# Performance work log

Measured on AMD Instinct MI355X. Metric: run time of the kernel, lower is better.

The kernel has to match this reference:

```python
import jax, jax.numpy as jnp
import numpy as np

DIM = 1024
NUM_HEADS = 16
HEAD_DIM = DIM // NUM_HEADS
SCALE = HEAD_DIM ** -0.5


def setup_inputs() -> dict:
    key = jax.random.key(0)
    k1, k2, k3, k4 = jax.random.split(key, 4)
    x = jax.random.normal(k1, (4, 2048, DIM), dtype=jnp.float32)
    # torch nn.Linear(dim, 3*dim, bias=False): weight shape [3*dim, dim]
    w_qkv = jax.random.normal(k2, (3 * DIM, DIM), dtype=jnp.float32) * (DIM ** -0.5)
    # torch nn.Linear(dim, dim): weight [dim, dim], bias [dim]
    w_proj = jax.random.normal(k3, (DIM, DIM), dtype=jnp.float32) * (DIM ** -0.5)
    b_proj = jax.random.normal(k4, (DIM,), dtype=jnp.float32) * 0.01
    return {"x": x, "w_qkv": w_qkv, "w_proj": w_proj, "b_proj": b_proj}


def reference(x, w_qkv, w_proj, b_proj):
    B, N, C = x.shape
    # qkv: [B, N, 3*C] -> [3, B, H, N, Dh]
    qkv = (x @ w_qkv.T).reshape(B, N, 3, NUM_HEADS, HEAD_DIM)
    qkv = jnp.transpose(qkv, (2, 0, 3, 1, 4))
    q, k, v = qkv[0], qkv[1], qkv[2]
    # full score matrix, as in the original module
    attn = jnp.einsum("bhqd,bhkd->bhqk", q, k) * SCALE
    attn = jax.nn.softmax(attn, axis=-1)
    out = jnp.einsum("bhqk,bhkd->bhqd", attn, v)  # [B,H,N,Dh]
    out = jnp.transpose(out, (0, 2, 1, 3)).reshape(B, N, C)
    return out @ w_proj.T + b_proj
```

## Files before the change

kernel.cpp:

```cpp
#include <hip/hip_runtime.h>
#include <stdint.h>

#define DIM 1024
#define SEQ 2048
#define BATCH 4
#define ROWS (BATCH*SEQ)
#define QSCALE 0.1803368801111f

typedef __attribute__((ext_vector_type(8))) short bf16x8;
typedef __attribute__((ext_vector_type(4))) float f32x4;

#if __has_builtin(__builtin_amdgcn_exp2f)
#define EXP2F(x) __builtin_amdgcn_exp2f(x)
#else
#define EXP2F(x) __expf((x) * 0.69314718056f)
#endif

__device__ __forceinline__ unsigned short f2bf(float f) {
  union { float f; unsigned int u; } v; v.f = f;
  unsigned int u = v.u;
  return (unsigned short)((u + 0x7FFFu + ((u >> 16) & 1u)) >> 16);
}

__device__ __forceinline__ unsigned int pack_bf16_trunc(float lo, float hi) {
  union { float f; unsigned int u; } a, b;
  a.f = lo; b.f = hi;
  return __builtin_amdgcn_perm(b.u, a.u, 0x07060302u);
}

__device__ __forceinline__ void gload_lds16(const void* g, void* l) {
  __builtin_amdgcn_global_load_lds(
      (const __attribute__((address_space(1))) unsigned int*)g,
      (__attribute__((address_space(3))) unsigned int*)l,
      16, 0, 0);
}

__global__ void cast_f32_bf16(const float* __restrict__ src,
                              unsigned short* __restrict__ dst, int n) {
  int i = (blockIdx.x * blockDim.x + threadIdx.x) * 4;
  if (i < n) {
    float4 f = *(const float4*)(src + i);
    ushort4 o;
    o.x = f2bf(f.x); o.y = f2bf(f.y); o.z = f2bf(f.z); o.w = f2bf(f.w);
    *(ushort4*)(dst + i) = o;
  }
}

__global__ __launch_bounds__(256) void gemm_qkv(
    const unsigned short* __restrict__ A,
    const unsigned short* __restrict__ W,
    unsigned short* __restrict__ qb,
    unsigned short* __restrict__ kb,
    unsigned short* __restrict__ vtb) {
  const int K = DIM;
  __shared__ unsigned short Al[128 * 32];
  __shared__ unsigned short Wl[128 * 32];
  const int tid  = threadIdx.x;
  const int wave = tid >> 6, lane = tid & 63;
  const int quad = lane >> 4, l16 = lane & 15;
  const int m0 = blockIdx.y * 128, n0 = blockIdx.x * 128;
  const int wr = (wave >> 1) * 64, wc = (wave & 1) * 64;
  const int which = n0 >> 10;

  f32x4 acc[4][4];
#pragma unroll
  for (int i = 0; i < 4; i++)
#pragma unroll
    for (int j = 0; j < 4; j++) acc[i][j] = (f32x4)0.f;

  const int arow = wave * 16 + (lane >> 2);
  const int acol = (lane & 3) * 8;
  const unsigned short* Ag = A + (size_t)(m0 + arow) * K + acol;
  const unsigned short* Wg = W + (size_t)(n0 + arow) * K + acol;

  if (which < 2) {
    for (int kt = 0; kt < K; kt += 32) {
      __syncthreads();
#pragma unroll
      for (int i = 0; i < 2; i++) {
        gload_lds16((const void*)(Ag + (size_t)(i * 64) * K + kt), (void*)&Al[i * 2048 + wave * 512]);
        gload_lds16((const void*)(Wg + (size_t)(i * 64) * K + kt), (void*)&Wl[i * 2048 + wave * 512]);
      }
      __syncthreads();
      bf16x8 af[4], wf[4];
#pragma unroll
      for (int i = 0; i < 4; i++) {
        af[i] = *(const bf16x8*)&Al[(wr + i * 16 + l16) * 32 + quad * 8];
        wf[i] = *(const bf16x8*)&Wl[(wc + i * 16 + l16) * 32 + quad * 8];
      }
#pragma unroll
      for (int i = 0; i < 4; i++)
#pragma unroll
        for (int j = 0; j < 4; j++)
          acc[i][j] = __builtin_amdgcn_mfma_f32_16x16x32_bf16(wf[j], af[i], acc[i][j], 0, 0, 0);
    }
    const float sc = (which == 0) ? QSCALE : 1.f;
    unsigned short* base = (which == 0) ? qb : kb;
#pragma unroll
    for (int i = 0; i < 4; i++) {
      const int tok = m0 + wr + i * 16 + l16;
      const int b = tok >> 11, n = tok & 2047;
#pragma unroll
      for (int j = 0; j < 4; j++) {
        const int col0 = n0 + wc + j * 16 + quad * 4;
        const int h = (col0 >> 6) & 15, d = col0 & 63;
        ushort4 o4;
        o4.x = f2bf(acc[i][j][0] * sc); o4.y = f2bf(acc[i][j][1] * sc);
        o4.z = f2bf(acc[i][j][2] * sc); o4.w = f2bf(acc[i][j][3] * sc);
        *(ushort4*)&base[((size_t)(b * 16 + h) * SEQ + n) * 64 + d] = o4;
      }
    }
  } else {
    for (int kt = 0; kt < K; kt += 32) {
      __syncthreads();
#pragma unroll
      for (int i = 0; i < 2; i++) {
        gload_lds16((const void*)(Ag + (size_t)(i * 64) * K + kt), (void*)&Al[i * 2048 + wave * 512]);
        gload_lds16((const void*)(Wg + (size_t)(i * 64) * K + kt), (void*)&Wl[i * 2048 + wave * 512]);
      }
      __syncthreads();
      bf16x8 af[4], wf[4];
#pragma unroll
      for (int i = 0; i < 4; i++) {
        af[i] = *(const bf16x8*)&Al[(wr + i * 16 + l16) * 32 + quad * 8];
        wf[i] = *(const bf16x8*)&Wl[(wc + i * 16 + l16) * 32 + quad * 8];
      }
#pragma unroll
      for (int i = 0; i < 4; i++)
#pragma unroll
        for (int j = 0; j < 4; j++)
          acc[i][j] = __builtin_amdgcn_mfma_f32_16x16x32_bf16(af[i], wf[j], acc[i][j], 0, 0, 0);
    }
#pragma unroll
    for (int i = 0; i < 4; i++) {
      const int row = m0 + wr + i * 16 + quad * 4;
      const int b = row >> 11, n = row & 2047;
#pragma unroll
      for (int j = 0; j < 4; j++) {
        const int col = n0 + wc + j * 16 + l16;
        const int h = (col >> 6) & 15, d = col & 63;
        ushort4 o4;
        o4.x = f2bf(acc[i][j][0]); o4.y = f2bf(acc[i][j][1]);
        o4.z = f2bf(acc[i][j][2]); o4.w = f2bf(acc[i][j][3]);
        *(ushort4*)&vtb[((size_t)(b * 16 + h) * 64 + d) * SEQ + n] = o4;
      }
    }
  }
}

__global__ __launch_bounds__(256, 2) void attn_kernel(
    const unsigned short* __restrict__ qb,
    const unsigned short* __restrict__ kb,
    const unsigned short* __restrict__ vtb,
    unsigned short* __restrict__ out) {
  __shared__ unsigned short Kl[2][64 * 64];
  __shared__ unsigned short Vl[2][64 * 64];
  __shared__ unsigned short Pb[4][64 * 64];

  const int tid  = threadIdx.x;
  const int wave = tid >> 6, lane = tid & 63;
  const int quad = lane >> 4, l16 = lane & 15;
  const int qtile = blockIdx.x;
  const int bh    = blockIdx.y;
  const size_t qkbase = (size_t)bh * SEQ * 64;
  const int q0 = qtile * 256 + wave * 64;

  bf16x8 qf[4][2];
#pragma unroll
  for (int mi = 0; mi < 4; mi++)
#pragma unroll
    for (int kk = 0; kk < 2; kk++)
      qf[mi][kk] = *(const bf16x8*)&qb[qkbase + (size_t)(q0 + mi * 16 + l16) * 64 + kk * 32 + quad * 8];

  f32x4 o[4][4];
#pragma unroll
  for (int mi = 0; mi < 4; mi++)
#pragma unroll
    for (int nt = 0; nt < 4; nt++) o[mi][nt] = (f32x4)0.f;
  f32x4 lacc[4];
#pragma unroll
  for (int mi = 0; mi < 4; mi++) lacc[mi] = (f32x4)0.f;

  bf16x8 ones;
#pragma unroll
  for (int j = 0; j < 8; j++) ones[j] = (short)0x3F80;

  const unsigned short* Kg = kb + qkbase;
  const unsigned short* Vg = vtb + (size_t)bh * 64 * SEQ;
  const int srow = tid >> 3;
  const int schk = tid & 7;

  auto stage = [&](int kt, int buf) {
#pragma unroll
    for (int p = 0; p < 2; p++) {
      const int r = p * 32 + srow;
      const int sw = schk ^ (r & 7);
      gload_lds16((const void*)(Kg + (size_t)(kt + r) * 64 + sw * 8),
                  (void*)&Kl[buf][p * 2048 + wave * 512]);
      gload_lds16((const void*)(Vg + (size_t)r * SEQ + kt + sw * 8),
                  (void*)&Vl[buf][p * 2048 + wave * 512]);
    }
  };

  stage(0, 0);

  int buf = 0;
  for (int kt = 0; kt < SEQ; kt += 64, buf ^= 1) {
    __syncthreads();
    if (kt + 64 < SEQ) stage(kt + 64, buf ^ 1);

#pragma unroll
    for (int nh = 0; nh < 4; nh++) {
      const int R = nh * 16 + l16;
      const int sb = R & 7;
      bf16x8 kf0 = *(const bf16x8*)&Kl[buf][R * 64 + ((quad ^ sb) << 3)];
      bf16x8 kf1 = *(const bf16x8*)&Kl[buf][R * 64 + (((4 + quad) ^ sb) << 3)];
#pragma unroll
      for (int mi = 0; mi < 4; mi++) {
        f32x4 s = (f32x4)0.f;
        s = __builtin_amdgcn_mfma_f32_16x16x32_bf16(kf0, qf[mi][0], s, 0, 0, 0);
        s = __builtin_amdgcn_mfma_f32_16x16x32_bf16(kf1, qf[mi][1], s, 0, 0, 0);
        const float e0 = EXP2F(s[0]), e1 = EXP2F(s[1]);
        const float e2 = EXP2F(s[2]), e3 = EXP2F(s[3]);
        uint2 pk;
        pk.x = pack_bf16_trunc(e0, e1);
        pk.y = pack_bf16_trunc(e2, e3);
        const int q = mi * 16 + l16;
        const int chunk = (nh * 2 + (quad >> 1)) ^ (l16 & 7);
        *(uint2*)&Pb[wave][q * 64 + (chunk << 3) + ((quad & 1) << 2)] = pk;
      }
    }

#pragma unroll
    for (int kk = 0; kk < 2; kk++) {
      bf16x8 vf[4];
#pragma unroll
      for (int nt = 0; nt < 4; nt++) {
        const int R = nt * 16 + l16;
        vf[nt] = *(const bf16x8*)&Vl[buf][R * 64 + (((kk * 4 + quad) ^ (R & 7)) << 3)];
      }
#pragma unroll
      for (int mi = 0; mi < 4; mi++) {
        const int R = mi * 16 + l16;
        bf16x8 pf = *(const bf16x8*)&Pb[wave][R * 64 + (((kk * 4 + quad) ^ (l16 & 7)) << 3)];
        lacc[mi] = __builtin_amdgcn_mfma_f32_16x16x32_bf16(pf, ones, lacc[mi], 0, 0, 0);
#pragma unroll
        for (int nt = 0; nt < 4; nt++)
          o[mi][nt] = __builtin_amdgcn_mfma_f32_16x16x32_bf16(pf, vf[nt], o[mi][nt], 0, 0, 0);
      }
    }
  }

  const int h = bh & 15, b = bh >> 4;
#pragma unroll
  for (int mi = 0; mi < 4; mi++) {
    float inv[4];
#pragma unroll
    for (int r = 0; r < 4; r++) inv[r] = 1.f / lacc[mi][r];
#pragma unroll
    for (int nt = 0; nt < 4; nt++)
#pragma unroll
      for (int r = 0; r < 4; r++)
        out[((size_t)(b * SEQ + q0 + mi * 16 + quad * 4 + r)) * DIM + h * 64 + nt * 16 + l16] =
            f2bf(o[mi][nt][r] * inv[r]);
  }
}

__global__ __launch_bounds__(256) void gemm_proj(
    const unsigned short* __restrict__ A,
    const unsigned short* __restrict__ W,
    float* __restrict__ out,
    const float* __restrict__ bias) {
  const int N = DIM, K = DIM;
  __shared__ unsigned short Al[128 * 32];
  __shared__ unsigned short Wl[128 * 32];
  const int tid  = threadIdx.x;
  const int wave = tid >> 6, lane = tid & 63;
  const int quad = lane >> 4, l16 = lane & 15;
  const int m0 = blockIdx.y * 128, n0 = blockIdx.x * 128;
  const int wr = (wave >> 1) * 64, wc = (wave & 1) * 64;

  f32x4 acc[4][4];
#pragma unroll
  for (int i = 0; i < 4; i++)
#pragma unroll
    for (int j = 0; j < 4; j++) acc[i][j] = (f32x4)0.f;

  const int arow = wave * 16 + (lane >> 2);
  const int acol = (lane & 3) * 8;
  const unsigned short* Ag = A + (size_t)(m0 + arow) * K + acol;
  const unsigned short* Wg = W + (size_t)(n0 + arow) * K + acol;

  for (int kt = 0; kt < K; kt += 32) {
    __syncthreads();
#pragma unroll
    for (int i = 0; i < 2; i++) {
      gload_lds16((const void*)(Ag + (size_t)(i * 64) * K + kt), (void*)&Al[i * 2048 + wave * 512]);
      gload_lds16((const void*)(Wg + (size_t)(i * 64) * K + kt), (void*)&Wl[i * 2048 + wave * 512]);
    }
    __syncthreads();

    bf16x8 af[4], wf[4];
#pragma unroll
    for (int i = 0; i < 4; i++) {
      af[i] = *(const bf16x8*)&Al[(wr + i * 16 + l16) * 32 + quad * 8];
      wf[i] = *(const bf16x8*)&Wl[(wc + i * 16 + l16) * 32 + quad * 8];
    }
#pragma unroll
    for (int i = 0; i < 4; i++)
#pragma unroll
      for (int j = 0; j < 4; j++)
        acc[i][j] = __builtin_amdgcn_mfma_f32_16x16x32_bf16(af[i], wf[j], acc[i][j], 0, 0, 0);
  }

#pragma unroll
  for (int i = 0; i < 4; i++) {
    const int row = m0 + wr + i * 16 + quad * 4;
#pragma unroll
    for (int j = 0; j < 4; j++) {
      const int col = n0 + wc + j * 16 + l16;
      const float bv = bias[col];
#pragma unroll
      for (int r = 0; r < 4; r++)
        out[(size_t)(row + r) * N + col] = acc[i][j][r] + bv;
    }
  }
}

extern "C" void kernel_launch(void* const* d_in, const int* in_sizes, int n_in,
                              void* d_out, int out_size, void* d_ws, size_t ws_size,
                              hipStream_t stream) {
  const float* x      = (const float*)d_in[0];
  const float* w_qkv  = (const float*)d_in[1];
  const float* w_proj = (const float*)d_in[2];
  const float* b_proj = (const float*)d_in[3];
  float* outp = (float*)d_out;

  char* ws = (char*)d_ws;
  unsigned short* xb     = (unsigned short*)(ws);
  unsigned short* wqkvb  = (unsigned short*)(ws + (16u << 20));
  unsigned short* wprojb = (unsigned short*)(ws + (22u << 20));
  unsigned short* qb     = (unsigned short*)(ws + (24u << 20));
  unsigned short* kb     = (unsigned short*)(ws + (40u << 20));
  unsigned short* vtb    = (unsigned short*)(ws + (56u << 20));
  unsigned short* aout   = (unsigned short*)(ws + (72u << 20));

  cast_f32_bf16<<<ROWS * DIM / 1024, 256, 0, stream>>>(x, xb, ROWS * DIM);
  cast_f32_bf16<<<3 * DIM * DIM / 1024, 256, 0, stream>>>(w_qkv, wqkvb, 3 * DIM * DIM);
  cast_f32_bf16<<<DIM * DIM / 1024, 256, 0, stream>>>(w_proj, wprojb, DIM * DIM);

  gemm_qkv<<<dim3(24, 64), 256, 0, stream>>>(xb, wqkvb, qb, kb, vtb);
  attn_kernel<<<dim3(8, 64), 256, 0, stream>>>(qb, kb, vtb, aout);
  gemm_proj<<<dim3(8, 64), 256, 0, stream>>>(aout, wprojb, outp, b_proj);
}
```

Before: 266.2 us.

## Keep softmax probabilities in registers via fp16 MFMA and merge cast kernels

The attention kernel now feeds exp'd scores straight from the QK^T accumulator layout into 16x16x16 fp16 MFMAs for PV and the row sum, which removes the per-wave LDS P buffer and its store/load round trip. To make this work, V is stored as fp16 instead of bf16, and probabilities are packed with cvt_pkrtz. The three f32-to-bf16 cast launches are merged into one kernel. In exchange the PV MFMAs use half the K depth, so twice as many instructions are issued, and fp16 may overflow for large V values.

Result: slower. 281.0 us (+5.5%).

```diff
diff --git a/kernel.cpp b/kernel.cpp
--- a/kernel.cpp
+++ b/kernel.cpp
@@ -9,6 +9,8 @@
 
 typedef __attribute__((ext_vector_type(8))) short bf16x8;
 typedef __attribute__((ext_vector_type(4))) float f32x4;
+typedef __attribute__((ext_vector_type(4))) _Float16 f16x4;
+typedef __attribute__((ext_vector_type(2))) __fp16 fp16x2_raw;
 
 #if __has_builtin(__builtin_amdgcn_exp2f)
 #define EXP2F(x) __builtin_amdgcn_exp2f(x)
@@ -16,16 +18,24 @@
 #define EXP2F(x) __expf((x) * 0.69314718056f)
 #endif
 
+#define MFMA16x16(a,b,c) __builtin_amdgcn_mfma_f32_16x16x16f16(a,b,c,0,0,0)
+
 __device__ __forceinline__ unsigned short f2bf(float f) {
   union { float f; unsigned int u; } v; v.f = f;
   unsigned int u = v.u;
   return (unsigned short)((u + 0x7FFFu + ((u >> 16) & 1u)) >> 16);
 }
 
-__device__ __forceinline__ unsigned int pack_bf16_trunc(float lo, float hi) {
-  union { float f; unsigned int u; } a, b;
-  a.f = lo; b.f = hi;
-  return __builtin_amdgcn_perm(b.u, a.u, 0x07060302u);
+__device__ __forceinline__ unsigned short f2h(float f) {
+  union { _Float16 h; unsigned short u; } v;
+  v.h = (_Float16)f;
+  return v.u;
+}
+
+__device__ __forceinline__ unsigned int pkrtz_bits(float lo, float hi) {
+  union { fp16x2_raw h; unsigned int u; } v;
+  v.h = __builtin_amdgcn_cvt_pkrtz(lo, hi);
+  return v.u;
 }
 
 __device__ __forceinline__ void gload_lds16(const void* g, void* l) {
@@ -35,15 +45,23 @@
       16, 0, 0);
 }
 
-__global__ void cast_f32_bf16(const float* __restrict__ src,
-                              unsigned short* __restrict__ dst, int n) {
-  int i = (blockIdx.x * blockDim.x + threadIdx.x) * 4;
-  if (i < n) {
-    float4 f = *(const float4*)(src + i);
-    ushort4 o;
-    o.x = f2bf(f.x); o.y = f2bf(f.y); o.z = f2bf(f.z); o.w = f2bf(f.w);
-    *(ushort4*)(dst + i) = o;
-  }
+__global__ void cast_all(const float* __restrict__ x,
+                         const float* __restrict__ wq,
+                         const float* __restrict__ wp,
+                         unsigned short* __restrict__ xb,
+                         unsigned short* __restrict__ wqb,
+                         unsigned short* __restrict__ wpb) {
+  const int i = (blockIdx.x * blockDim.x + threadIdx.x) * 4;
+  const float* src;
+  unsigned short* dst;
+  int off;
+  if (i < ROWS * DIM)                 { src = x;  dst = xb;  off = i; }
+  else if (i < ROWS * DIM + 3 * DIM * DIM) { src = wq; dst = wqb; off = i - ROWS * DIM; }
+  else                                { src = wp; dst = wpb; off = i - ROWS * DIM - 3 * DIM * DIM; }
+  float4 f = *(const float4*)(src + off);
+  ushort4 o;
+  o.x = f2bf(f.x); o.y = f2bf(f.y); o.z = f2bf(f.z); o.w = f2bf(f.w);
+  *(ushort4*)(dst + off) = o;
 }
 
 __global__ __launch_bounds__(256) void gemm_qkv(
@@ -140,8 +158,8 @@
         const int col = n0 + wc + j * 16 + l16;
         const int h = (col >> 6) & 15, d = col & 63;
         ushort4 o4;
-        o4.x = f2bf(acc[i][j][0]); o4.y = f2bf(acc[i][j][1]);
-        o4.z = f2bf(acc[i][j][2]); o4.w = f2bf(acc[i][j][3]);
+        o4.x = f2h(acc[i][j][0]); o4.y = f2h(acc[i][j][1]);
+        o4.z = f2h(acc[i][j][2]); o4.w = f2h(acc[i][j][3]);
         *(ushort4*)&vtb[((size_t)(b * 16 + h) * 64 + d) * SEQ + n] = o4;
       }
     }
@@ -155,7 +173,6 @@
     unsigned short* __restrict__ out) {
   __shared__ unsigned short Kl[2][64 * 64];
   __shared__ unsigned short Vl[2][64 * 64];
-  __shared__ unsigned short Pb[4][64 * 64];
 
   const int tid  = threadIdx.x;
   const int wave = tid >> 6, lane = tid & 63;
@@ -181,9 +198,8 @@
 #pragma unroll
   for (int mi = 0; mi < 4; mi++) lacc[mi] = (f32x4)0.f;
 
-  bf16x8 ones;
-#pragma unroll
-  for (int j = 0; j < 8; j++) ones[j] = (short)0x3F80;
+  union { f16x4 v; unsigned int d[2]; } ones;
+  ones.d[0] = 0x3C003C00u; ones.d[1] = 0x3C003C00u;
 
   const unsigned short* Kg = kb + qkbase;
   const unsigned short* Vg = vtb + (size_t)bh * 64 * SEQ;
@@ -215,38 +231,25 @@
       const int sb = R & 7;
       bf16x8 kf0 = *(const bf16x8*)&Kl[buf][R * 64 + ((quad ^ sb) << 3)];
       bf16x8 kf1 = *(const bf16x8*)&Kl[buf][R * 64 + (((4 + quad) ^ sb) << 3)];
+      f16x4 vf[4];
+#pragma unroll
+      for (int nt = 0; nt < 4; nt++) {
+        const int vr = nt * 16 + l16;
+        const int c = nh * 2 + (quad >> 1);
+        vf[nt] = *(const f16x4*)&Vl[buf][vr * 64 + (((c ^ (vr & 7)) << 3) | ((quad & 1) << 2))];
+      }
 #pragma unroll
       for (int mi = 0; mi < 4; mi++) {
         f32x4 s = (f32x4)0.f;
         s = __builtin_amdgcn_mfma_f32_16x16x32_bf16(kf0, qf[mi][0], s, 0, 0, 0);
         s = __builtin_amdgcn_mfma_f32_16x16x32_bf16(kf1, qf[mi][1], s, 0, 0, 0);
-        const float e0 = EXP2F(s[0]), e1 = EXP2F(s[1]);
-        const float e2 = EXP2F(s[2]), e3 = EXP2F(s[3]);
-        uint2 pk;
-        pk.x = pack_bf16_trunc(e0, e1);
-        pk.y = pack_bf16_trunc(e2, e3);
-        const int q = mi * 16 + l16;
-        const int chunk = (nh * 2 + (quad >> 1)) ^ (l16 & 7);
-        *(uint2*)&Pb[wave][q * 64 + (chunk << 3) + ((quad & 1) << 2)] = pk;
-      }
-    }
-
-#pragma unroll
-    for (int kk = 0; kk < 2; kk++) {
-      bf16x8 vf[4];
-#pragma unroll
-      for (int nt = 0; nt < 4; nt++) {
-        const int R = nt * 16 + l16;
-        vf[nt] = *(const bf16x8*)&Vl[buf][R * 64 + (((kk * 4 + quad) ^ (R & 7)) << 3)];
-      }
-#pragma unroll
-      for (int mi = 0; mi < 4; mi++) {
-        const int R = mi * 16 + l16;
-        bf16x8 pf = *(const bf16x8*)&Pb[wave][R * 64 + (((kk * 4 + quad) ^ (l16 & 7)) << 3)];
-        lacc[mi] = __builtin_amdgcn_mfma_f32_16x16x32_bf16(pf, ones, lacc[mi], 0, 0, 0);
+        union { f16x4 v; unsigned int d[2]; } pu;
+        pu.d[0] = pkrtz_bits(EXP2F(s[0]), EXP2F(s[1]));
+        pu.d[1] = pkrtz_bits(EXP2F(s[2]), EXP2F(s[3]));
+        lacc[mi] = MFMA16x16(pu.v, ones.v, lacc[mi]);
 #pragma unroll
         for (int nt = 0; nt < 4; nt++)
-          o[mi][nt] = __builtin_amdgcn_mfma_f32_16x16x32_bf16(pf, vf[nt], o[mi][nt], 0, 0, 0);
+          o[mi][nt] = MFMA16x16(pu.v, vf[nt], o[mi][nt]);
       }
     }
   }
@@ -345,9 +348,8 @@
   unsigned short* vtb    = (unsigned short*)(ws + (56u << 20));
   unsigned short* aout   = (unsigned short*)(ws + (72u << 20));
 
-  cast_f32_bf16<<<ROWS * DIM / 1024, 256, 0, stream>>>(x, xb, ROWS * DIM);
-  cast_f32_bf16<<<3 * DIM * DIM / 1024, 256, 0, stream>>>(w_qkv, wqkvb, 3 * DIM * DIM);
-  cast_f32_bf16<<<DIM * DIM / 1024, 256, 0, stream>>>(w_proj, wprojb, DIM * DIM);
+  const int total4 = (ROWS * DIM + 3 * DIM * DIM + DIM * DIM) / 4;
+  cast_all<<<total4 / 256, 256, 0, stream>>>(x, w_qkv, w_proj, xb, wqkvb, wprojb);
 
   gemm_qkv<<<dim3(24, 64), 256, 0, stream>>>(xb, wqkvb, qb, kb, vtb);
   attn_kernel<<<dim3(8, 64), 256, 0, stream>>>(qb, kb, vtb, aout);
```
